# Kernel optimization log

Measured on AMD Instinct MI355X. Metric: run time of the kernel, lower is better.

Reference implementation:

```python
import jax, jax.numpy as jnp
import numpy as np

IN_F, OUT_F, BATCH = 4096, 11008, 8

def setup_inputs() -> dict:
    key = jax.random.key(0)
    k_x, k_s, k_sg, k_b = jax.random.split(key, 4)
    x = jax.random.normal(k_x, (BATCH, IN_F), dtype=jnp.float32)
    # stored codes in [1, 255] as in QINSCodec.encode (uint8 storage)
    stored = jax.random.randint(k_s, (OUT_F, IN_F), 1, 256, dtype=jnp.int32).astype(jnp.uint8)
    # sign in {-1, +1} (int8 storage)
    sign = (jax.random.randint(k_sg, (OUT_F, IN_F), 0, 2, dtype=jnp.int32) * 2 - 1).astype(jnp.int8)
    log_min = jnp.array([-10.0], dtype=jnp.float32)
    log_max = jnp.array([0.0], dtype=jnp.float32)
    bias = jax.random.normal(k_b, (OUT_F,), dtype=jnp.float32) * 0.02
    return {"x": x, "stored": stored, "sign": sign, "log_min": log_min, "log_max": log_max, "bias": bias}

def _decode(stored, sign, log_min, log_max):
    # QINSCodec.decode: normalized = (255 - stored)/254; w = sign * exp(log_min + normalized*(log_max-log_min))
    normalized = (255.0 - stored.astype(jnp.float32)) / 254.0
    log_w = log_min + normalized * (log_max - log_min)
    return sign.astype(jnp.float32) * jnp.exp(log_w)

def reference(x, stored, sign, log_min, log_max, bias):
    lmin = log_min[0]
    lmax = log_max[0]
    w = _decode(stored, sign, lmin, lmax)            # [OUT_F, IN_F]
    return x @ w.T + bias                            # F.linear(x, w, bias)
```

## Files before the change

kernel.cpp:

```cpp
#include <hip/hip_runtime.h>
#include <stdint.h>

#define IN_F   4096
#define OUT_F  11008
#define BATCH  8
#define RPW    4
#define WAVES  2
#define RPB    (RPW*WAVES)
#define CHUNK  256

__device__ __forceinline__ float qins_decode(int code, int sgn, float d0, float d1) {
    const float e = __builtin_amdgcn_exp2f(fmaf((float)code, d1, d0));
    const uint32_t m = ((uint32_t)sgn) & 0x80000000u;
    return __uint_as_float(__float_as_uint(e) ^ m);
}

__global__ __launch_bounds__(WAVES*64, 4)
void qins_linear_kernel(const float* __restrict__ x,
                        const int*   __restrict__ stored,
                        const int*   __restrict__ sign,
                        const float* __restrict__ log_min,
                        const float* __restrict__ log_max,
                        const float* __restrict__ bias,
                        float* __restrict__ out)
{
    const int lane = threadIdx.x & 63;
    const int wave = threadIdx.x >> 6;
    const int o0   = blockIdx.x * RPB + wave * RPW;

    const float lmin = log_min[0];
    const float lmax = log_max[0];
    const float L2E  = 1.44269504088896340736f;
    const float d1 = -(lmax - lmin) * (L2E / 254.0f);
    const float d0 = (lmin + (lmax - lmin) * (255.0f / 254.0f)) * L2E;

    float acc[RPW][BATCH];
#pragma unroll
    for (int r = 0; r < RPW; ++r)
#pragma unroll
        for (int b = 0; b < BATCH; ++b) acc[r][b] = 0.0f;

    const int ii0 = lane * 4;

    for (int i0 = 0; i0 < IN_F; i0 += CHUNK) {
        const int ii = i0 + ii0;

        float4 xr[BATCH];
#pragma unroll
        for (int b = 0; b < BATCH; ++b)
            xr[b] = *reinterpret_cast<const float4*>(x + b * IN_F + ii);

        int4 sc[RPW], sg[RPW];
#pragma unroll
        for (int r = 0; r < RPW; ++r) {
            const size_t off = (size_t)(o0 + r) * IN_F + ii;
            sc[r] = *reinterpret_cast<const int4*>(stored + off);
            sg[r] = *reinterpret_cast<const int4*>(sign + off);
        }

#pragma unroll
        for (int r = 0; r < RPW; ++r) {
            const float w0 = qins_decode(sc[r].x, sg[r].x, d0, d1);
            const float w1 = qins_decode(sc[r].y, sg[r].y, d0, d1);
            const float w2 = qins_decode(sc[r].z, sg[r].z, d0, d1);
            const float w3 = qins_decode(sc[r].w, sg[r].w, d0, d1);
#pragma unroll
            for (int b = 0; b < BATCH; ++b) {
                float a = acc[r][b];
                a = fmaf(w0, xr[b].x, a);
                a = fmaf(w1, xr[b].y, a);
                a = fmaf(w2, xr[b].z, a);
                a = fmaf(w3, xr[b].w, a);
                acc[r][b] = a;
            }
        }
    }

#pragma unroll
    for (int r = 0; r < RPW; ++r)
#pragma unroll
        for (int b = 0; b < BATCH; ++b) {
            float v = acc[r][b];
#pragma unroll
            for (int s = 32; s >= 1; s >>= 1)
                v += __shfl_xor(v, s, 64);
            acc[r][b] = v;
        }

    if (lane == 0) {
#pragma unroll
        for (int r = 0; r < RPW; ++r) {
            const float bv = bias[o0 + r];
#pragma unroll
            for (int b = 0; b < BATCH; ++b)
                out[(size_t)b * OUT_F + o0 + r] = acc[r][b] + bv;
        }
    }
}

extern "C" void kernel_launch(void* const* d_in, const int* in_sizes, int n_in,
                              void* d_out, int out_size, void* d_ws, size_t ws_size,
                              hipStream_t stream)
{
    const float* x      = (const float*)d_in[0];
    const int*   stored = (const int*)d_in[1];
    const int*   sign   = (const int*)d_in[2];
    const float* lmin   = (const float*)d_in[3];
    const float* lmax   = (const float*)d_in[4];
    const float* bias   = (const float*)d_in[5];
    float* out = (float*)d_out;

    dim3 grid(OUT_F / RPB), block(WAVES * 64);
    qins_linear_kernel<<<grid, block, 0, stream>>>(x, stored, sign, lmin, lmax, bias, out);
}
```

Baseline: 81.64 us.

## Restructure GEMV to 2 rows per wave with 16 contiguous elements per lane

Rows per wave drop from 4 to 2 and waves per block rise from 2 to 4, keeping 8 rows per block. Each lane now covers 16 contiguous input elements per 1024-wide chunk as four int4 loads, instead of 4 elements per 256-wide chunk, and x is loaded inside the inner loop. The aim is fewer loop iterations and more independent wide loads in flight per lane, to better saturate HBM bandwidth on the int32 stored/sign streams. The trade-off is strided per-lane access (64B apart across lanes), which may hurt coalescing. It also adds int-typed row offsets.

```diff
diff --git a/kernel.cpp b/kernel.cpp
--- a/kernel.cpp
+++ b/kernel.cpp
@@ -4,10 +4,10 @@
 #define IN_F   4096
 #define OUT_F  11008
 #define BATCH  8
-#define RPW    4
-#define WAVES  2
+#define RPW    2
+#define WAVES  4
 #define RPB    (RPW*WAVES)
-#define CHUNK  256
+#define CHUNK  1024
 
 __device__ __forceinline__ float qins_decode(int code, int sgn, float d0, float d1) {
     const float e = __builtin_amdgcn_exp2f(fmaf((float)code, d1, d0));
@@ -40,38 +40,41 @@
 #pragma unroll
         for (int b = 0; b < BATCH; ++b) acc[r][b] = 0.0f;
 
-    const int ii0 = lane * 4;
+    const int lb    = lane * 16;
+    const int row0  = (o0 + 0) * IN_F + lb;
+    const int row1  = (o0 + 1) * IN_F + lb;
 
-    for (int i0 = 0; i0 < IN_F; i0 += CHUNK) {
-        const int ii = i0 + ii0;
+#pragma unroll 1
+    for (int c = 0; c < IN_F; c += CHUNK) {
+#pragma unroll
+        for (int j = 0; j < 4; ++j) {
+            const int ip = c + 4 * j;
+            const int4 c0 = *reinterpret_cast<const int4*>(stored + row0 + ip);
+            const int4 c1 = *reinterpret_cast<const int4*>(stored + row1 + ip);
+            const int4 g0 = *reinterpret_cast<const int4*>(sign + row0 + ip);
+            const int4 g1 = *reinterpret_cast<const int4*>(sign + row1 + ip);
 
-        float4 xr[BATCH];
-#pragma unroll
-        for (int b = 0; b < BATCH; ++b)
-            xr[b] = *reinterpret_cast<const float4*>(x + b * IN_F + ii);
-
-        int4 sc[RPW], sg[RPW];
-#pragma unroll
-        for (int r = 0; r < RPW; ++r) {
-            const size_t off = (size_t)(o0 + r) * IN_F + ii;
-            sc[r] = *reinterpret_cast<const int4*>(stored + off);
-            sg[r] = *reinterpret_cast<const int4*>(sign + off);
-        }
+            const float w00 = qins_decode(c0.x, g0.x, d0, d1);
+            const float w01 = qins_decode(c0.y, g0.y, d0, d1);
+            const float w02 = qins_decode(c0.z, g0.z, d0, d1);
+            const float w03 = qins_decode(c0.w, g0.w, d0, d1);
+            const float w10 = qins_decode(c1.x, g1.x, d0, d1);
+            const float w11 = qins_decode(c1.y, g1.y, d0, d1);
+            const float w12 = qins_decode(c1.z, g1.z, d0, d1);
+            const float w13 = qins_decode(c1.w, g1.w, d0, d1);
 
 #pragma unroll
-        for (int r = 0; r < RPW; ++r) {
-            const float w0 = qins_decode(sc[r].x, sg[r].x, d0, d1);
-            const float w1 = qins_decode(sc[r].y, sg[r].y, d0, d1);
-            const float w2 = qins_decode(sc[r].z, sg[r].z, d0, d1);
-            const float w3 = qins_decode(sc[r].w, sg[r].w, d0, d1);
-#pragma unroll
             for (int b = 0; b < BATCH; ++b) {
-                float a = acc[r][b];
-                a = fmaf(w0, xr[b].x, a);
-                a = fmaf(w1, xr[b].y, a);
-                a = fmaf(w2, xr[b].z, a);
-                a = fmaf(w3, xr[b].w, a);
-                acc[r][b] = a;
+                const float4 t = *reinterpret_cast<const float4*>(
+                    x + b * IN_F + ip + lb);
+                float a0 = acc[0][b];
+                float a1 = acc[1][b];
+                a0 = fmaf(w00, t.x, a0); a1 = fmaf(w10, t.x, a1);
+                a0 = fmaf(w01, t.y, a0); a1 = fmaf(w11, t.y, a1);
+                a0 = fmaf(w02, t.z, a0); a1 = fmaf(w12, t.z, a1);
+                a0 = fmaf(w03, t.w, a0); a1 = fmaf(w13, t.w, a1);
+                acc[0][b] = a0;
+                acc[1][b] = a1;
             }
         }
     }
```

After: 131.3 us. +60.8%, slower.
